# Kernel optimization log

Measured on AMD Instinct MI355X. Metric: run time of the kernel, lower is better.

The kernel has to match this reference:

```python
import jax, jax.numpy as jnp
import numpy as np

B, EMB, P, K = 8192, 768, 96, 256
D = EMB // P  # dsub = 8


def setup_inputs() -> dict:
    key = jax.random.key(0)
    k1, k2 = jax.random.split(key)
    vecs = jax.random.normal(k1, (B, EMB), dtype=jnp.float32)
    # torch init: uniform(-1, 1)
    codebook = jax.random.uniform(k2, (P, K, D), dtype=jnp.float32, minval=-1.0, maxval=1.0)
    return {"vecs": vecs, "codebook": codebook}


def reference(vecs, codebook):
    b = vecs.shape[0]
    p, k, d = codebook.shape
    v = vecs.reshape(b, p, d)                                  # [B,P,D]
    # squared distances via expanded quadratic (avoids [B,P,K,D] broadcast):
    # ||v-c||^2 = ||v||^2 - 2 v.c + ||c||^2
    dots = jnp.einsum('bpd,pkd->bpk', v, codebook)             # [B,P,K]
    d2 = (jnp.sum(v * v, axis=-1, keepdims=True)               # [B,P,1]
          - 2.0 * dots
          + jnp.sum(codebook * codebook, axis=-1)[None])       # [1,P,K]
    proba = jax.nn.softmax(-d2, axis=-1)                       # [B,P,K]
    # straight-through hard assignment
    idx = jnp.argmax(proba, axis=-1)                           # [B,P]
    hard = jax.nn.one_hot(idx, k, dtype=proba.dtype)           # [B,P,K]
    ste = jax.lax.stop_gradient(hard - proba) + proba
    # reconstruct from codebook
    out = jnp.einsum('bpk,pkd->bpd', ste, codebook).reshape(b, p * d)
    return out
```

## Files before the change

kernel.cpp:

```cpp
#include <hip/hip_runtime.h>


typedef float f32x4  __attribute__((ext_vector_type(4)));
typedef short bf16x8 __attribute__((ext_vector_type(8)));

namespace {
constexpr int kB   = 8192;
constexpr int kEMB = 768;
constexpr int kP   = 96;
constexpr int kK   = 256;
constexpr int kD   = 8;
constexpr int QPB  = 64;
}

#define PQ_THR 2.0e-3f

__device__ __forceinline__ short bf16_rn(float x)
{
    unsigned u = __float_as_uint(x);
    unsigned r = u + 0x7FFFu + ((u >> 16) & 1u);
    return (short)(r >> 16);
}
__device__ __forceinline__ float bf16_f32(short s)
{
    return __uint_as_float(((unsigned)(unsigned short)s) << 16);
}

__device__ __forceinline__ float dpp_max16(float x)
{
    int y;
    y = __builtin_amdgcn_update_dpp(__float_as_int(x), __float_as_int(x),
                                    0xB1, 0xF, 0xF, true);
    x = fmaxf(x, __int_as_float(y));
    y = __builtin_amdgcn_update_dpp(__float_as_int(x), __float_as_int(x),
                                    0x4E, 0xF, 0xF, true);
    x = fmaxf(x, __int_as_float(y));
    y = __builtin_amdgcn_update_dpp(__float_as_int(x), __float_as_int(x),
                                    0x141, 0xF, 0xF, true);
    x = fmaxf(x, __int_as_float(y));
    y = __builtin_amdgcn_update_dpp(__float_as_int(x), __float_as_int(x),
                                    0x140, 0xF, 0xF, true);
    x = fmaxf(x, __int_as_float(y));
    return x;
}

__device__ __forceinline__ int dpp_min16(int x)
{
    int y;
    y = __builtin_amdgcn_update_dpp(x, x, 0xB1, 0xF, 0xF, true);
    x = min(x, y);
    y = __builtin_amdgcn_update_dpp(x, x, 0x4E, 0xF, 0xF, true);
    x = min(x, y);
    y = __builtin_amdgcn_update_dpp(x, x, 0x141, 0xF, 0xF, true);
    x = min(x, y);
    y = __builtin_amdgcn_update_dpp(x, x, 0x140, 0xF, 0xF, true);
    x = min(x, y);
    return x;
}

template <int I>
__device__ __forceinline__ int rescore_pick(float Mi, const f32x4 (&acc)[16],
                                            int colq, const float* vq,
                                            const float* code_f,
                                            const float* h_f)
{
    float bs = -__builtin_inff();
    int   bk = 1024;
#pragma unroll
    for (int m = 0; m < 16; ++m) {
        const float a = acc[m][I];
        if (a >= Mi - PQ_THR) {
            const int kc = m * 16 + colq;
            const float* cr = &code_f[kc * kD];
            float s = fmaf(cr[0], vq[0], h_f[kc]);
            s = fmaf(cr[1], vq[1], s);
            s = fmaf(cr[2], vq[2], s);
            s = fmaf(cr[3], vq[3], s);
            s = fmaf(cr[4], vq[4], s);
            s = fmaf(cr[5], vq[5], s);
            s = fmaf(cr[6], vq[6], s);
            s = fmaf(cr[7], vq[7], s);
            if (s > bs) {
                bs = s;
                bk = kc;
            }
        }
    }
    const float S = dpp_max16(bs);
    return dpp_min16((bs == S) ? bk : 1024);
}

__global__ __launch_bounds__(256, 4)
void pq_mfma_kernel(const float* __restrict__ vecs,
                    const float* __restrict__ codebook,
                    float* __restrict__ out)
{
    __shared__ alignas(16) short lds_B[16 * 512];
    __shared__ alignas(16) float lds_code[kK * kD];
    __shared__ alignas(16) float lds_h[kK];
    __shared__ alignas(16) float lds_v[QPB][kD];

    const int p = blockIdx.y;
    const int t = threadIdx.x;
    const int l = t & 63;
    const int colq = l & 15;
    const int hi   = l >> 4;
    const int w    = t >> 6;

    {
        const f32x4* cb4 =
            reinterpret_cast<const f32x4*>(codebook + (size_t)p * kK * kD);
        f32x4 ca = cb4[2 * t];
        f32x4 cbv = cb4[2 * t + 1];
        float cc[8] = {ca.x, ca.y, ca.z, ca.w, cbv.x, cbv.y, cbv.z, cbv.w};
        bf16x8 ph, pm;
        float c2 = 0.0f;
#pragma unroll
        for (int j = 0; j < 8; ++j) {
            float x  = cc[j];
            short h  = bf16_rn(x);
            short m_ = bf16_rn(x - bf16_f32(h));
            ph[j] = h; pm[j] = m_;
            c2 = fmaf(x, x, c2);
        }
        lds_h[t] = -0.5f * c2;
        f32x4* rc = reinterpret_cast<f32x4*>(&lds_code[t * kD]);
        rc[0] = ca;
        rc[1] = cbv;
        const int tile = t >> 4, col = t & 15;
        short* bp = &lds_B[tile * 512 + col * 8];
        *reinterpret_cast<bf16x8*>(bp + 0 * 128) = ph;
        *reinterpret_cast<bf16x8*>(bp + 1 * 128) = pm;
        *reinterpret_cast<bf16x8*>(bp + 2 * 128) = ph;
        *reinterpret_cast<bf16x8*>(bp + 3 * 128) = pm;
    }

    const int qrow = blockIdx.x * QPB + w * 16 + colq;
    bf16x8 a0;
    {
        const float* vp = vecs + (size_t)qrow * kEMB + p * kD;
        f32x4 va = *reinterpret_cast<const f32x4*>(vp);
        f32x4 vb = *reinterpret_cast<const f32x4*>(vp + 4);
        if (hi == 0) {
            f32x4* rv = reinterpret_cast<f32x4*>(&lds_v[w * 16 + colq][0]);
            rv[0] = va;
            rv[1] = vb;
        }
        float vv[8] = {va.x, va.y, va.z, va.w, vb.x, vb.y, vb.z, vb.w};
#pragma unroll
        for (int j = 0; j < 8; ++j) {
            float x  = vv[j];
            short h  = bf16_rn(x);
            short m_ = bf16_rn(x - bf16_f32(h));
            a0[j] = (hi < 2) ? h : m_;
        }
    }

    __syncthreads();

    f32x4 acc[16];
    const f32x4 z4 = {0.0f, 0.0f, 0.0f, 0.0f};
    const short* bbase = &lds_B[l * 8];
#pragma unroll
    for (int m = 0; m < 16; ++m) {
        bf16x8 b0 = *reinterpret_cast<const bf16x8*>(bbase + m * 512);
        acc[m] = __builtin_amdgcn_mfma_f32_16x16x32_bf16(a0, b0, z4, 0, 0, 0);
    }

    const float NEG = -__builtin_inff();
    float M0 = NEG, M1 = NEG, M2 = NEG, M3 = NEG;
#pragma unroll
    for (int m = 0; m < 16; ++m) {
        const float hm = lds_h[m * 16 + colq];
        acc[m].x += hm; acc[m].y += hm; acc[m].z += hm; acc[m].w += hm;
        M0 = fmaxf(M0, acc[m].x);
        M1 = fmaxf(M1, acc[m].y);
        M2 = fmaxf(M2, acc[m].z);
        M3 = fmaxf(M3, acc[m].w);
    }
    M0 = dpp_max16(M0); M1 = dpp_max16(M1);
    M2 = dpp_max16(M2); M3 = dpp_max16(M3);

    const float* vq0 = &lds_v[w * 16 + hi * 4 + 0][0];
    const float* vq1 = &lds_v[w * 16 + hi * 4 + 1][0];
    const float* vq2 = &lds_v[w * 16 + hi * 4 + 2][0];
    const float* vq3 = &lds_v[w * 16 + hi * 4 + 3][0];
    const int k0 = rescore_pick<0>(M0, acc, colq, vq0, lds_code, lds_h);
    const int k1 = rescore_pick<1>(M1, acc, colq, vq1, lds_code, lds_h);
    const int k2 = rescore_pick<2>(M2, acc, colq, vq2, lds_code, lds_h);
    const int k3 = rescore_pick<3>(M3, acc, colq, vq3, lds_code, lds_h);

    if (colq < 8) {
        const int ka = (colq & 2) ? k1 : k0;
        const int kb = (colq & 2) ? k3 : k2;
        const int kq = (colq & 4) ? kb : ka;
        const int row = blockIdx.x * QPB + w * 16 + (hi << 2) + (colq >> 1);
        const f32x4* cr = reinterpret_cast<const f32x4*>(
            codebook + ((size_t)p * kK + kq) * kD) + (colq & 1);
        f32x4* op = reinterpret_cast<f32x4*>(
            out + (size_t)row * kEMB + p * kD) + (colq & 1);
        *op = *cr;
    }
}

extern "C" void kernel_launch(void* const* d_in, const int* in_sizes, int n_in,
                              void* d_out, int out_size, void* d_ws, size_t ws_size,
                              hipStream_t stream)
{
    const float* vecs     = (const float*)d_in[0];
    const float* codebook = (const float*)d_in[1];
    float* out            = (float*)d_out;

    dim3 grid(kB / QPB, kP, 1);
    dim3 block(256, 1, 1);
    hipLaunchKernelGGL(pq_mfma_kernel, grid, block, 0, stream,
                       vecs, codebook, out);
}
```

Measured before the change: 131.8 us.

## Use 3-way bf16 split MFMA with top-2 margin test to skip fp32 rescoring

Splits the operands into high, mid and low bf16 parts and issues two MFMAs per tile, folding the -0.5||c||^2 bias into the accumulator init. This tightens the approximate scores enough to lower the near-tie threshold. The candidate scan becomes a per-row top-2 search merged across lanes with DPP, and the fp32 rescore now runs only when the top-2 margin falls below the threshold. The rescore reads the query and codebook straight from global memory, so the LDS copies of code and vecs go away, and an XOR swizzle is added to the B tile layout. The cost is twice as many MFMAs, extra work converting the split parts, and a risk of wrong argmax if the error bound does not hold.

New measurement: 143.5 us. 1.09x slower.

```diff
diff --git a/kernel.cpp b/kernel.cpp
--- a/kernel.cpp
+++ b/kernel.cpp
@@ -13,7 +13,7 @@
 constexpr int QPB  = 64;
 }
 
-#define PQ_THR 2.0e-3f
+#define PQ_THR 4.0e-5f
 
 __device__ __forceinline__ short bf16_rn(float x)
 {
@@ -58,36 +58,67 @@
     return x;
 }
 
+template <int CTRL>
+__device__ __forceinline__ void merge_step(float& t1, float& t2, int& idx)
+{
+    const float y1 = __int_as_float(__builtin_amdgcn_update_dpp(
+        __float_as_int(t1), __float_as_int(t1), CTRL, 0xF, 0xF, true));
+    const float y2 = __int_as_float(__builtin_amdgcn_update_dpp(
+        __float_as_int(t2), __float_as_int(t2), CTRL, 0xF, 0xF, true));
+    const int yi = __builtin_amdgcn_update_dpp(idx, idx, CTRL, 0xF, 0xF, true);
+    const bool gt = y1 > t1;
+    t2 = fmaxf(fminf(t1, y1), fmaxf(t2, y2));
+    t1 = fmaxf(t1, y1);
+    idx = gt ? yi : idx;
+}
+
 template <int I>
-__device__ __forceinline__ int rescore_pick(float Mi, const f32x4 (&acc)[16],
-                                            int colq, const float* vq,
-                                            const float* code_f,
-                                            const float* h_f)
-{
-    float bs = -__builtin_inff();
-    int   bk = 1024;
-#pragma unroll
-    for (int m = 0; m < 16; ++m) {
-        const float a = acc[m][I];
-        if (a >= Mi - PQ_THR) {
+__device__ __forceinline__ int decide(const f32x4 (&acc)[16], int colq,
+                                      const float* vrow0, const float* cb_p,
+                                      const float* h_lds)
+{
+    float t1 = acc[0][I];
+    float t2 = -__builtin_inff();
+    int   idx = colq;
+#pragma unroll
+    for (int m = 1; m < 16; ++m) {
+        const float v = acc[m][I];
+        const bool gt = v > t1;
+        t2 = fmaxf(fminf(v, t1), t2);
+        t1 = fmaxf(t1, v);
+        idx = gt ? ((m * 16) | colq) : idx;
+    }
+    merge_step<0xB1>(t1, t2, idx);
+    merge_step<0x4E>(t1, t2, idx);
+    merge_step<0x141>(t1, t2, idx);
+    merge_step<0x140>(t1, t2, idx);
+
+    if (t1 - t2 <= PQ_THR) {
+        const float* vq = vrow0 + I * kEMB;
+        const f32x4 va = *reinterpret_cast<const f32x4*>(vq);
+        const f32x4 vb = *reinterpret_cast<const f32x4*>(vq + 4);
+        float bs = -__builtin_inff();
+        int   bk = 1024;
+#pragma unroll
+        for (int m = 0; m < 16; ++m) {
             const int kc = m * 16 + colq;
-            const float* cr = &code_f[kc * kD];
-            float s = fmaf(cr[0], vq[0], h_f[kc]);
-            s = fmaf(cr[1], vq[1], s);
-            s = fmaf(cr[2], vq[2], s);
-            s = fmaf(cr[3], vq[3], s);
-            s = fmaf(cr[4], vq[4], s);
-            s = fmaf(cr[5], vq[5], s);
-            s = fmaf(cr[6], vq[6], s);
-            s = fmaf(cr[7], vq[7], s);
-            if (s > bs) {
-                bs = s;
-                bk = kc;
-            }
-        }
-    }
-    const float S = dpp_max16(bs);
-    return dpp_min16((bs == S) ? bk : 1024);
+            const f32x4* cr = reinterpret_cast<const f32x4*>(cb_p + kc * kD);
+            const f32x4 c0 = cr[0];
+            const f32x4 c1 = cr[1];
+            float s = fmaf(c0.x, va.x, h_lds[kc]);
+            s = fmaf(c0.y, va.y, s);
+            s = fmaf(c0.z, va.z, s);
+            s = fmaf(c0.w, va.w, s);
+            s = fmaf(c1.x, vb.x, s);
+            s = fmaf(c1.y, vb.y, s);
+            s = fmaf(c1.z, vb.z, s);
+            s = fmaf(c1.w, vb.w, s);
+            if (s > bs) { bs = s; bk = kc; }
+        }
+        const float S = dpp_max16(bs);
+        idx = dpp_min16((bs == S) ? bk : 1024);
+    }
+    return idx;
 }
 
 __global__ __launch_bounds__(256, 4)
@@ -95,10 +126,8 @@
                     const float* __restrict__ codebook,
                     float* __restrict__ out)
 {
-    __shared__ alignas(16) short lds_B[16 * 512];
-    __shared__ alignas(16) float lds_code[kK * kD];
+    __shared__ alignas(16) short lds_B[16 * 2 * 512];
     __shared__ alignas(16) float lds_h[kK];
-    __shared__ alignas(16) float lds_v[QPB][kD];
 
     const int p = blockIdx.y;
     const int t = threadIdx.x;
@@ -107,88 +136,80 @@
     const int hi   = l >> 4;
     const int w    = t >> 6;
 
+    const float* cb_p = codebook + (size_t)p * kK * kD;
+
     {
-        const f32x4* cb4 =
-            reinterpret_cast<const f32x4*>(codebook + (size_t)p * kK * kD);
+        const f32x4* cb4 = reinterpret_cast<const f32x4*>(cb_p);
         f32x4 ca = cb4[2 * t];
         f32x4 cbv = cb4[2 * t + 1];
         float cc[8] = {ca.x, ca.y, ca.z, ca.w, cbv.x, cbv.y, cbv.z, cbv.w};
-        bf16x8 ph, pm;
+        bf16x8 ph, pm, pl;
         float c2 = 0.0f;
 #pragma unroll
         for (int j = 0; j < 8; ++j) {
             float x  = cc[j];
             short h  = bf16_rn(x);
-            short m_ = bf16_rn(x - bf16_f32(h));
-            ph[j] = h; pm[j] = m_;
+            float d1 = x - bf16_f32(h);
+            short m_ = bf16_rn(d1);
+            short lo = bf16_rn(d1 - bf16_f32(m_));
+            ph[j] = h; pm[j] = m_; pl[j] = lo;
             c2 = fmaf(x, x, c2);
         }
         lds_h[t] = -0.5f * c2;
-        f32x4* rc = reinterpret_cast<f32x4*>(&lds_code[t * kD]);
-        rc[0] = ca;
-        rc[1] = cbv;
         const int tile = t >> 4, col = t & 15;
-        short* bp = &lds_B[tile * 512 + col * 8];
-        *reinterpret_cast<bf16x8*>(bp + 0 * 128) = ph;
-        *reinterpret_cast<bf16x8*>(bp + 1 * 128) = pm;
-        *reinterpret_cast<bf16x8*>(bp + 2 * 128) = ph;
-        *reinterpret_cast<bf16x8*>(bp + 3 * 128) = pm;
+        const int swz = (tile & 3) << 4;
+#pragma unroll
+        for (int g = 0; g < 4; ++g) {
+            const bf16x8 v0 = (g & 1) ? pm : ph;
+            const bf16x8 v1 = (g == 0 || g == 2) ? pl : ((g == 1) ? ph : pm);
+            *reinterpret_cast<bf16x8*>(
+                &lds_B[(((tile * 2 + 0) * 512) + g * 128 + col * 8) ^ swz]) = v0;
+            *reinterpret_cast<bf16x8*>(
+                &lds_B[(((tile * 2 + 1) * 512) + g * 128 + col * 8) ^ swz]) = v1;
+        }
     }
 
     const int qrow = blockIdx.x * QPB + w * 16 + colq;
-    bf16x8 a0;
+    bf16x8 a0, a1;
     {
         const float* vp = vecs + (size_t)qrow * kEMB + p * kD;
         f32x4 va = *reinterpret_cast<const f32x4*>(vp);
         f32x4 vb = *reinterpret_cast<const f32x4*>(vp + 4);
-        if (hi == 0) {
-            f32x4* rv = reinterpret_cast<f32x4*>(&lds_v[w * 16 + colq][0]);
-            rv[0] = va;
-            rv[1] = vb;
-        }
         float vv[8] = {va.x, va.y, va.z, va.w, vb.x, vb.y, vb.z, vb.w};
 #pragma unroll
         for (int j = 0; j < 8; ++j) {
             float x  = vv[j];
             short h  = bf16_rn(x);
-            short m_ = bf16_rn(x - bf16_f32(h));
+            float d1 = x - bf16_f32(h);
+            short m_ = bf16_rn(d1);
+            short lo = bf16_rn(d1 - bf16_f32(m_));
             a0[j] = (hi < 2) ? h : m_;
+            a1[j] = (hi == 0) ? h : ((hi == 2) ? m_ : lo);
         }
     }
 
     __syncthreads();
 
     f32x4 acc[16];
-    const f32x4 z4 = {0.0f, 0.0f, 0.0f, 0.0f};
-    const short* bbase = &lds_B[l * 8];
 #pragma unroll
     for (int m = 0; m < 16; ++m) {
-        bf16x8 b0 = *reinterpret_cast<const bf16x8*>(bbase + m * 512);
-        acc[m] = __builtin_amdgcn_mfma_f32_16x16x32_bf16(a0, b0, z4, 0, 0, 0);
-    }
-
-    const float NEG = -__builtin_inff();
-    float M0 = NEG, M1 = NEG, M2 = NEG, M3 = NEG;
-#pragma unroll
-    for (int m = 0; m < 16; ++m) {
-        const float hm = lds_h[m * 16 + colq];
-        acc[m].x += hm; acc[m].y += hm; acc[m].z += hm; acc[m].w += hm;
-        M0 = fmaxf(M0, acc[m].x);
-        M1 = fmaxf(M1, acc[m].y);
-        M2 = fmaxf(M2, acc[m].z);
-        M3 = fmaxf(M3, acc[m].w);
-    }
-    M0 = dpp_max16(M0); M1 = dpp_max16(M1);
-    M2 = dpp_max16(M2); M3 = dpp_max16(M3);
-
-    const float* vq0 = &lds_v[w * 16 + hi * 4 + 0][0];
-    const float* vq1 = &lds_v[w * 16 + hi * 4 + 1][0];
-    const float* vq2 = &lds_v[w * 16 + hi * 4 + 2][0];
-    const float* vq3 = &lds_v[w * 16 + hi * 4 + 3][0];
-    const int k0 = rescore_pick<0>(M0, acc, colq, vq0, lds_code, lds_h);
-    const int k1 = rescore_pick<1>(M1, acc, colq, vq1, lds_code, lds_h);
-    const int k2 = rescore_pick<2>(M2, acc, colq, vq2, lds_code, lds_h);
-    const int k3 = rescore_pick<3>(M3, acc, colq, vq3, lds_code, lds_h);
+        const int swz = (m & 3) << 4;
+        const bf16x8 b0 = *reinterpret_cast<const bf16x8*>(
+            &lds_B[(((m * 2 + 0) * 512) + l * 8) ^ swz]);
+        const bf16x8 b1 = *reinterpret_cast<const bf16x8*>(
+            &lds_B[(((m * 2 + 1) * 512) + l * 8) ^ swz]);
+        const float hb = lds_h[m * 16 + colq];
+        const f32x4 hc = {hb, hb, hb, hb};
+        f32x4 t0 = __builtin_amdgcn_mfma_f32_16x16x32_bf16(a0, b0, hc, 0, 0, 0);
+        acc[m]   = __builtin_amdgcn_mfma_f32_16x16x32_bf16(a1, b1, t0, 0, 0, 0);
+    }
+
+    const float* vrow0 = vecs +
+        (size_t)(blockIdx.x * QPB + w * 16 + hi * 4) * kEMB + p * kD;
+    const int k0 = decide<0>(acc, colq, vrow0, cb_p, lds_h);
+    const int k1 = decide<1>(acc, colq, vrow0, cb_p, lds_h);
+    const int k2 = decide<2>(acc, colq, vrow0, cb_p, lds_h);
+    const int k3 = decide<3>(acc, colq, vrow0, cb_p, lds_h);
 
     if (colq < 8) {
         const int ka = (colq & 2) ? k1 : k0;
@@ -196,7 +217,7 @@
         const int kq = (colq & 4) ? kb : ka;
         const int row = blockIdx.x * QPB + w * 16 + (hi << 2) + (colq >> 1);
         const f32x4* cr = reinterpret_cast<const f32x4*>(
-            codebook + ((size_t)p * kK + kq) * kD) + (colq & 1);
+            cb_p + (size_t)kq * kD) + (colq & 1);
         f32x4* op = reinterpret_cast<f32x4*>(
             out + (size_t)row * kEMB + p * kD) + (colq & 1);
         *op = *cr;
```
